# Performance work log

Hardware: AMD Instinct MI355X
Metric: run time of the kernel (lower is better)

The kernel has to match this reference:

```python
import jax, jax.numpy as jnp
import numpy as np

N = 10000      # num_nodes
E = 640000     # num_edges
IN = 512       # in_channels
H = 7          # GCNConv hidden/out dim (hard-coded in module)


def _glorot(key, shape):
    s = np.sqrt(6.0 / (shape[0] + shape[1])).astype(np.float32)
    return jax.random.uniform(key, shape, jnp.float32, -s, s)


def setup_inputs() -> dict:
    key = jax.random.key(0)
    k = jax.random.split(key, 6)
    x = jax.random.normal(k[0], (N, IN), jnp.float32)
    edge_index = jax.random.randint(k[1], (2, E), 0, N, dtype=jnp.int32)
    edge_attr = jax.random.uniform(k[2], (E, 1), jnp.float32)
    adj = jnp.zeros((N, N), jnp.float32)  # unused by forward, per original API
    W1 = _glorot(k[3], (IN, H))
    b1 = jnp.zeros((H,), jnp.float32)
    W2 = _glorot(k[4], (H, H))
    b2 = jnp.zeros((H,), jnp.float32)
    return {"x": x, "edge_index": edge_index, "edge_attr": edge_attr,
            "adj": adj, "W1": W1, "b1": b1, "W2": W2, "b2": b2}


def _gcn_layer(x, row, col, ew, W, b):
    n = x.shape[0]
    # add self-loops (improved=False -> loop weight 1)
    loop = jnp.arange(n, dtype=row.dtype)
    row_f = jnp.concatenate([row, loop])
    col_f = jnp.concatenate([col, loop])
    ew_f = jnp.concatenate([ew, jnp.ones((n,), x.dtype)])
    # symmetric degree normalization: deg from scatter_add on row
    deg = jax.ops.segment_sum(ew_f, row_f, num_segments=n)
    deg_inv = jnp.where(deg > 0, deg ** -0.5, 0.0).astype(x.dtype)
    norm = deg_inv[row_f] * ew_f * deg_inv[col_f]          # [E+N]
    h = x @ W                                              # [n, out]
    out = jax.ops.segment_sum(norm[:, None] * h[col_f], row_f, num_segments=n)
    return out + b


def reference(x, edge_index, edge_attr, adj, W1, b1, W2, b2):
    row, col = edge_index[0], edge_index[1]
    ew = edge_attr.reshape(-1)
    h = _gcn_layer(x, row, col, ew, W1, b1)
    h = _gcn_layer(h, row, col, ew, W2, b2)
    reg = jnp.zeros((1,), x.dtype)
    return h, reg
```

## Files before the change

kernel.cpp:

```cpp
#include <hip/hip_runtime.h>

#define NN   10000
#define NE   640000
#define IC   512
#define H    7
#define HP   8
#define NCH  256
#define CE   (NE / NCH)
#define RG   250
#define RN   40
#define CAP  3072
#define MMB  256
#define GN   32
#define NGB  ((NN + GN - 1) / GN)

__device__ __forceinline__ float wave_sum(float v) {
    #pragma unroll
    for (int off = 32; off; off >>= 1) v += __shfl_xor(v, off);
    return v;
}

__device__ __forceinline__ float group16_sum(float v) {
    #pragma unroll
    for (int off = 1; off < 16; off <<= 1) v += __shfl_xor(v, off);
    return v;
}

__global__ __launch_bounds__(1024) void k_bucket_mm1(
    const int* __restrict__ row, const int* __restrict__ col,
    const float* __restrict__ ew, const float* __restrict__ x,
    const float* __restrict__ W1, int* __restrict__ ghist,
    int* __restrict__ goffs, int2* __restrict__ gbuf2,
    float* __restrict__ h1)
{
    __shared__ int   lhist[RG];
    __shared__ int   loffs[RG];
    __shared__ int   lcur[RG];
    __shared__ int2  st[CE];
    __shared__ float wls[IC * H];
    const int tid = threadIdx.x;

    if (blockIdx.x < NCH) {
        const int base = blockIdx.x * CE;
        if (tid < RG) lhist[tid] = 0;
        __syncthreads();
        int ex[3]; float ef[3];
        #pragma unroll
        for (int k = 0; k < 3; ++k) {
            const int i = tid + k * 1024;
            ex[k] = -1;
            if (i < CE) {
                const int e = base + i;
                const int r = row[e], c = col[e];
                const int rg = r / RN, rl = r - rg * RN;
                ex[k] = c | (rl << 14) | (rg << 20);
                ef[k] = ew[e];
                atomicAdd(&lhist[rg], 1);
            }
        }
        __syncthreads();
        if (tid < 64) {
            const int ln = tid;
            int t4[4]; int s4 = 0;
            #pragma unroll
            for (int k = 0; k < 4; ++k) {
                const int j = ln * 4 + k;
                t4[k] = (j < RG) ? lhist[j] : 0;
                s4 += t4[k];
            }
            int s = s4;
            #pragma unroll
            for (int off = 1; off < 64; off <<= 1) {
                const int t = __shfl_up(s, off);
                if (ln >= off) s += t;
            }
            int run = s - s4;
            #pragma unroll
            for (int k = 0; k < 4; ++k) {
                const int j = ln * 4 + k;
                if (j < RG) { loffs[j] = run; lcur[j] = run; }
                run += t4[k];
            }
        }
        __syncthreads();
        #pragma unroll
        for (int k = 0; k < 3; ++k) {
            if (ex[k] >= 0) {
                const int pos = atomicAdd(&lcur[ex[k] >> 20], 1);
                st[pos] = make_int2(ex[k], __float_as_int(ef[k]));
            }
        }
        __syncthreads();
        #pragma unroll
        for (int k = 0; k < 3; ++k) {
            const int i = tid + k * 1024;
            if (i < CE) gbuf2[base + i] = st[i];
        }
        if (tid < RG) {
            ghist[blockIdx.x * RG + tid] = lhist[tid];
            goffs[blockIdx.x * RG + tid] = loffs[tid];
        }
    } else {
        for (int i = tid; i < IC * H; i += 1024) wls[i] = W1[i];
        __syncthreads();
        const int wv = tid >> 6, ln = tid & 63;
        const int rb = (blockIdx.x - NCH) * RN;
        for (int r0 = wv; r0 < RN; r0 += 16) {
            const int r = rb + r0;
            if (r >= NN) break;
            const float4* xr4 = (const float4*)(x + (size_t)r * IC);
            const float4 a0 = xr4[ln * 2], a1 = xr4[ln * 2 + 1];
            const float e8[8] = {a0.x, a0.y, a0.z, a0.w, a1.x, a1.y, a1.z, a1.w};
            const float* wb = &wls[ln * 8 * H];
            float acc[H] = {};
            #pragma unroll
            for (int m = 0; m < 8; ++m)
                #pragma unroll
                for (int c = 0; c < H; ++c) acc[c] += e8[m] * wb[m * H + c];
            #pragma unroll
            for (int c = 0; c < H; ++c) {
                const float v = wave_sum(acc[c]);
                if (ln == 0) h1[r * HP + c] = v;
            }
            if (ln == 0) h1[r * HP + 7] = 0.0f;
        }
    }
}

__global__ __launch_bounds__(1024) void k_sort_deg_g1(
    const int* __restrict__ ghist, const int* __restrict__ goffs,
    const int2* __restrict__ gbuf2, const float* __restrict__ h1,
    float* __restrict__ dinv, float* __restrict__ g1,
    int2* __restrict__ nseg, int2* __restrict__ gbuf)
{
    __shared__ int2  staged[CAP];
    __shared__ int2  st2[CAP];
    __shared__ int   ccnt[NCH];
    __shared__ int   coff[NCH];
    __shared__ int   total_s;
    __shared__ int   lhist[RN];
    __shared__ float ldeg[RN];
    __shared__ int   loffs[RN];
    __shared__ int   lcur[RN];
    __shared__ float ldv[RN];
    const int tid = threadIdx.x, b = blockIdx.x;

    if (tid < NCH) ccnt[tid] = ghist[tid * RG + b];
    if (tid >= 256 && tid < 256 + RN) { lhist[tid - 256] = 0; ldeg[tid - 256] = 0.0f; }
    __syncthreads();
    if (tid < 64) {
        const int ln = tid;
        int t4[4]; int s4 = 0;
        #pragma unroll
        for (int k = 0; k < 4; ++k) { t4[k] = ccnt[ln * 4 + k]; s4 += t4[k]; }
        int s = s4;
        #pragma unroll
        for (int off = 1; off < 64; off <<= 1) {
            const int t = __shfl_up(s, off);
            if (ln >= off) s += t;
        }
        int run = s - s4;
        #pragma unroll
        for (int k = 0; k < 4; ++k) { coff[ln * 4 + k] = run; run += t4[k]; }
        if (ln == 63) total_s = run;
    }
    __syncthreads();
    {
        const int c = tid >> 2;
        const int cn = ccnt[c], co = coff[c];
        const int src = c * CE + goffs[c * RG + b];
        for (int i = tid & 3; i < cn; i += 4) staged[co + i] = gbuf2[src + i];
    }
    __syncthreads();
    const int cnt = total_s;
    int2 ed[3];
    #pragma unroll
    for (int k = 0; k < 3; ++k) {
        const int i = tid + k * 1024;
        ed[k] = make_int2(-1, 0);
        if (i < cnt) {
            ed[k] = staged[i];
            const int rl = (ed[k].x >> 14) & 63;
            atomicAdd(&lhist[rl], 1);
            atomicAdd(&ldeg[rl], __int_as_float(ed[k].y));
        }
    }
    __syncthreads();
    if (tid < 64) {
        int v = (tid < RN) ? lhist[tid] : 0;
        int s = v;
        #pragma unroll
        for (int off = 1; off < 64; off <<= 1) {
            const int t = __shfl_up(s, off);
            if (tid >= off) s += t;
        }
        if (tid < RN) { loffs[tid] = s - v; lcur[tid] = s - v; }
    } else if (tid >= 64 && tid < 64 + RN) {
        ldv[tid - 64] = rsqrtf(1.0f + ldeg[tid - 64]);
    }
    __syncthreads();
    #pragma unroll
    for (int k = 0; k < 3; ++k) {
        if (ed[k].x >= 0) {
            const int rl = (ed[k].x >> 14) & 63;
            const int pos = atomicAdd(&lcur[rl], 1);
            st2[pos] = ed[k];
        }
    }
    __syncthreads();
    #pragma unroll
    for (int k = 0; k < 3; ++k) {
        const int i = tid + k * 1024;
        if (i < cnt) gbuf[(size_t)b * CAP + i] = st2[i];
    }
    if (tid < RN) {
        dinv[b * RN + tid] = ldv[tid];
        nseg[b * RN + tid] = make_int2(loffs[tid], lhist[tid]);
    }
    if (tid < RN * HP) {
        const int n = tid >> 3;
        g1[(size_t)(b * RN) * HP + tid] = ldv[n] * h1[(size_t)(b * RN) * HP + tid];
    }
}

template <bool FUSE_MM2>
__global__ __launch_bounds__(512) void k_gather(
    const int2* __restrict__ gbuf, const int2* __restrict__ nseg,
    const float* __restrict__ dinv, const float* __restrict__ g,
    const float* __restrict__ bias, const float* __restrict__ W2,
    float* __restrict__ out)
{
    __shared__ float asum[GN][HP];
    __shared__ float vals[GN][HP];
    __shared__ float ldv[GN];
    __shared__ float w2[H * H];
    __shared__ float bb[H];
    const int tid = threadIdx.x, b = blockIdx.x;
    const int gid = tid >> 4, q = tid & 15;
    const int gn = b * GN + gid;
    if (!FUSE_MM2 && b == 0 && tid == 511) out[(size_t)NN * H] = 0.0f;
    if (tid < GN && b * GN + tid < NN) ldv[tid] = dinv[b * GN + tid];
    if (FUSE_MM2 && tid >= 64 && tid < 64 + H * H) w2[tid - 64] = W2[tid - 64];
    if (tid >= 128 && tid < 128 + H) bb[tid - 128] = bias[tid - 128];
    __syncthreads();
    if (gn < NN) {
        const int2 seg = nseg[gn];
        const int2* bk = gbuf + (size_t)(gn / RN) * CAP;
        const int kend = seg.x + seg.y;
        float acc[H] = {};
        for (int k = seg.x + q; k < kend; k += 32) {
            const int k2i = k + 16;
            const int2 e0 = bk[k];
            const int2 e1 = bk[k2i < kend ? k2i : k];
            const float w0 = __int_as_float(e0.y);
            const float w1 = (k2i < kend) ? __int_as_float(e1.y) : 0.0f;
            const float4* p0 = (const float4*)(g + (size_t)(e0.x & 16383) * HP);
            const float4* p1 = (const float4*)(g + (size_t)(e1.x & 16383) * HP);
            const float4 lo0 = p0[0], hi0 = p0[1];
            const float4 lo1 = p1[0], hi1 = p1[1];
            acc[0] += w0 * lo0.x + w1 * lo1.x;
            acc[1] += w0 * lo0.y + w1 * lo1.y;
            acc[2] += w0 * lo0.z + w1 * lo1.z;
            acc[3] += w0 * lo0.w + w1 * lo1.w;
            acc[4] += w0 * hi0.x + w1 * hi1.x;
            acc[5] += w0 * hi0.y + w1 * hi1.y;
            acc[6] += w0 * hi0.z + w1 * hi1.z;
        }
        #pragma unroll
        for (int j = 0; j < H; ++j) {
            const float s = group16_sum(acc[j]);
            if (q == 0) asum[gid][j] = s;
        }
    }
    __syncthreads();
    if (tid < GN * H) {
        const int n = tid / H, k = tid - n * H;
        const int node = b * GN + n;
        if (node < NN)
            vals[n][k] = ldv[n] * (asum[n][k] + g[(size_t)node * HP + k]) + bb[k];
    }
    __syncthreads();
    if (tid < GN * H) {
        const int n = tid / H, k = tid - n * H;
        const int node = b * GN + n;
        if (node < NN) {
            if (FUSE_MM2) {
                float o = 0.0f;
                #pragma unroll
                for (int j = 0; j < H; ++j) o += vals[n][j] * w2[j * H + k];
                out[(size_t)node * HP + k] = ldv[n] * o;
            } else {
                out[(size_t)node * H + k] = vals[n][k];
            }
        }
    }
    if (FUSE_MM2 && tid >= 256 && tid < 256 + GN) {
        const int node = b * GN + (tid - 256);
        if (node < NN) out[(size_t)node * HP + 7] = 0.0f;
    }
}

extern "C" void kernel_launch(void* const* d_in, const int* in_sizes, int n_in,
                              void* d_out, int out_size, void* d_ws, size_t ws_size,
                              hipStream_t stream) {
    const float* x  = (const float*)d_in[0];
    const int*   ei = (const int*)d_in[1];
    const float* ea = (const float*)d_in[2];
    const float* W1 = (const float*)d_in[4];
    const float* b1 = (const float*)d_in[5];
    const float* W2 = (const float*)d_in[6];
    const float* b2 = (const float*)d_in[7];
    float* out = (float*)d_out;

    char* p = (char*)d_ws;
    int* ghist = (int*)p;         p += sizeof(int) * NCH * RG;
    int* goffs = (int*)p;         p += sizeof(int) * NCH * RG;
    int2* gbuf2 = (int2*)p;       p += sizeof(int2) * NE;
    int2* gbuf = (int2*)p;        p += sizeof(int2) * RG * CAP;
    int2* nseg = (int2*)p;        p += sizeof(int2) * NN;
    float* h1 = (float*)p;        p += sizeof(float) * NN * HP;
    float* g1 = (float*)p;        p += sizeof(float) * NN * HP;
    float* g2 = (float*)p;        p += sizeof(float) * NN * HP;
    float* dinv = (float*)p;      p += sizeof(float) * NN;

    const int* row = ei;
    const int* col = ei + NE;

    k_bucket_mm1<<<NCH + MMB, 1024, 0, stream>>>(row, col, ea, x, W1,
                                                 ghist, goffs, gbuf2, h1);
    k_sort_deg_g1<<<RG, 1024, 0, stream>>>(ghist, goffs, gbuf2, h1,
                                           dinv, g1, nseg, gbuf);
    k_gather<true><<<NGB, 512, 0, stream>>>(gbuf, nseg, dinv, g1, b1, W2, g2);
    k_gather<false><<<NGB, 512, 0, stream>>>(gbuf, nseg, dinv, g2, b2, nullptr, out);
}
```

Baseline: 47.84 us.

## Move layer-1 matmul into sort kernel and pack edges as 32-bit col+fp16 weight

The x@W1 projection moves out of the bucketing kernel into the per-row-group sort kernel. Each block computes its 40 rows into shared memory and scales them by dinv directly, so the h1 global round trip goes away. The sorted edge buffer is packed into 32 bits (14-bit column plus fp16 weight) instead of int2, and staged memory is reused. This halves the edge bytes the two gather kernels read, at the cost of fp16 rounding of edge weights. It also serialises the matmul behind bucketing instead of running them concurrently.

```diff
diff --git a/kernel.cpp b/kernel.cpp
--- a/kernel.cpp
+++ b/kernel.cpp
@@ -1,4 +1,5 @@
 #include <hip/hip_runtime.h>
+#include <hip/hip_fp16.h>
 
 #define NN   10000
 #define NE   640000
@@ -10,7 +11,6 @@
 #define RG   250
 #define RN   40
 #define CAP  3072
-#define MMB  256
 #define GN   32
 #define NGB  ((NN + GN - 1) / GN)
 
@@ -26,88 +26,128 @@
     return v;
 }
 
-__global__ __launch_bounds__(1024) void k_bucket_mm1(
+__global__ __launch_bounds__(1024) void k_bucket(
     const int* __restrict__ row, const int* __restrict__ col,
-    const float* __restrict__ ew, const float* __restrict__ x,
-    const float* __restrict__ W1, int* __restrict__ ghist,
-    int* __restrict__ goffs, int2* __restrict__ gbuf2,
-    float* __restrict__ h1)
+    const float* __restrict__ ew, int* __restrict__ ghist,
+    int* __restrict__ goffs, int2* __restrict__ gbuf2)
 {
     __shared__ int   lhist[RG];
     __shared__ int   loffs[RG];
     __shared__ int   lcur[RG];
     __shared__ int2  st[CE];
+    const int tid = threadIdx.x;
+    const int base = blockIdx.x * CE;
+    if (tid < RG) lhist[tid] = 0;
+    __syncthreads();
+    int ex[3]; float ef[3];
+    #pragma unroll
+    for (int k = 0; k < 3; ++k) {
+        const int i = tid + k * 1024;
+        ex[k] = -1;
+        if (i < CE) {
+            const int e = base + i;
+            const int r = row[e], c = col[e];
+            const int rg = r / RN, rl = r - rg * RN;
+            ex[k] = c | (rl << 14) | (rg << 20);
+            ef[k] = ew[e];
+            atomicAdd(&lhist[rg], 1);
+        }
+    }
+    __syncthreads();
+    if (tid < 64) {
+        const int ln = tid;
+        int t4[4]; int s4 = 0;
+        #pragma unroll
+        for (int k = 0; k < 4; ++k) {
+            const int j = ln * 4 + k;
+            t4[k] = (j < RG) ? lhist[j] : 0;
+            s4 += t4[k];
+        }
+        int s = s4;
+        #pragma unroll
+        for (int off = 1; off < 64; off <<= 1) {
+            const int t = __shfl_up(s, off);
+            if (ln >= off) s += t;
+        }
+        int run = s - s4;
+        #pragma unroll
+        for (int k = 0; k < 4; ++k) {
+            const int j = ln * 4 + k;
+            if (j < RG) { loffs[j] = run; lcur[j] = run; }
+            run += t4[k];
+        }
+    }
+    __syncthreads();
+    #pragma unroll
+    for (int k = 0; k < 3; ++k) {
+        if (ex[k] >= 0) {
+            const int pos = atomicAdd(&lcur[ex[k] >> 20], 1);
+            st[pos] = make_int2(ex[k], __float_as_int(ef[k]));
+        }
+    }
+    __syncthreads();
+    #pragma unroll
+    for (int k = 0; k < 3; ++k) {
+        const int i = tid + k * 1024;
+        if (i < CE) gbuf2[base + i] = st[i];
+    }
+    if (tid < RG) {
+        ghist[blockIdx.x * RG + tid] = lhist[tid];
+        goffs[blockIdx.x * RG + tid] = loffs[tid];
+    }
+}
+
+__global__ __launch_bounds__(1024) void k_stage_sort_mm1(
+    const int* __restrict__ ghist, const int* __restrict__ goffs,
+    const int2* __restrict__ gbuf2, const float* __restrict__ x,
+    const float* __restrict__ W1, float* __restrict__ dinv,
+    float* __restrict__ g1, int2* __restrict__ nseg,
+    unsigned int* __restrict__ gbuf)
+{
+    __shared__ int2  staged[CAP];
     __shared__ float wls[IC * H];
-    const int tid = threadIdx.x;
-
-    if (blockIdx.x < NCH) {
-        const int base = blockIdx.x * CE;
-        if (tid < RG) lhist[tid] = 0;
-        __syncthreads();
-        int ex[3]; float ef[3];
-        #pragma unroll
-        for (int k = 0; k < 3; ++k) {
-            const int i = tid + k * 1024;
-            ex[k] = -1;
-            if (i < CE) {
-                const int e = base + i;
-                const int r = row[e], c = col[e];
-                const int rg = r / RN, rl = r - rg * RN;
-                ex[k] = c | (rl << 14) | (rg << 20);
-                ef[k] = ew[e];
-                atomicAdd(&lhist[rg], 1);
-            }
-        }
-        __syncthreads();
-        if (tid < 64) {
-            const int ln = tid;
-            int t4[4]; int s4 = 0;
-            #pragma unroll
-            for (int k = 0; k < 4; ++k) {
-                const int j = ln * 4 + k;
-                t4[k] = (j < RG) ? lhist[j] : 0;
-                s4 += t4[k];
-            }
-            int s = s4;
-            #pragma unroll
-            for (int off = 1; off < 64; off <<= 1) {
-                const int t = __shfl_up(s, off);
-                if (ln >= off) s += t;
-            }
-            int run = s - s4;
-            #pragma unroll
-            for (int k = 0; k < 4; ++k) {
-                const int j = ln * 4 + k;
-                if (j < RG) { loffs[j] = run; lcur[j] = run; }
-                run += t4[k];
-            }
-        }
-        __syncthreads();
-        #pragma unroll
-        for (int k = 0; k < 3; ++k) {
-            if (ex[k] >= 0) {
-                const int pos = atomicAdd(&lcur[ex[k] >> 20], 1);
-                st[pos] = make_int2(ex[k], __float_as_int(ef[k]));
-            }
-        }
-        __syncthreads();
-        #pragma unroll
-        for (int k = 0; k < 3; ++k) {
-            const int i = tid + k * 1024;
-            if (i < CE) gbuf2[base + i] = st[i];
-        }
-        if (tid < RG) {
-            ghist[blockIdx.x * RG + tid] = lhist[tid];
-            goffs[blockIdx.x * RG + tid] = loffs[tid];
-        }
-    } else {
-        for (int i = tid; i < IC * H; i += 1024) wls[i] = W1[i];
-        __syncthreads();
-        const int wv = tid >> 6, ln = tid & 63;
-        const int rb = (blockIdx.x - NCH) * RN;
+    __shared__ int   ccnt[NCH];
+    __shared__ int   coff[NCH];
+    __shared__ int   total_s;
+    __shared__ int   lhist[RN];
+    __shared__ float ldeg[RN];
+    __shared__ int   loffs[RN];
+    __shared__ int   lcur[RN];
+    __shared__ float ldv[RN];
+    __shared__ float htile[RN][HP];
+    const int tid = threadIdx.x, b = blockIdx.x;
+    const int wv = tid >> 6, ln = tid & 63;
+
+    if (tid < NCH) ccnt[tid] = ghist[tid * RG + b];
+    if (tid >= 256 && tid < 256 + RN) { lhist[tid - 256] = 0; ldeg[tid - 256] = 0.0f; }
+    for (int i = tid; i < IC * H; i += 1024) wls[i] = W1[i];
+    __syncthreads();
+    if (tid < 64) {
+        const int ln0 = tid;
+        int t4[4]; int s4 = 0;
+        #pragma unroll
+        for (int k = 0; k < 4; ++k) { t4[k] = ccnt[ln0 * 4 + k]; s4 += t4[k]; }
+        int s = s4;
+        #pragma unroll
+        for (int off = 1; off < 64; off <<= 1) {
+            const int t = __shfl_up(s, off);
+            if (ln0 >= off) s += t;
+        }
+        int run = s - s4;
+        #pragma unroll
+        for (int k = 0; k < 4; ++k) { coff[ln0 * 4 + k] = run; run += t4[k]; }
+        if (ln0 == 63) total_s = run;
+    }
+    __syncthreads();
+    {
+        const int c = tid >> 2;
+        const int cn = ccnt[c], co = coff[c];
+        const int src = c * CE + goffs[c * RG + b];
+        for (int i = tid & 3; i < cn; i += 4) staged[co + i] = gbuf2[src + i];
+    }
+    {
         for (int r0 = wv; r0 < RN; r0 += 16) {
-            const int r = rb + r0;
-            if (r >= NN) break;
+            const int r = b * RN + r0;
             const float4* xr4 = (const float4*)(x + (size_t)r * IC);
             const float4 a0 = xr4[ln * 2], a1 = xr4[ln * 2 + 1];
             const float e8[8] = {a0.x, a0.y, a0.z, a0.w, a1.x, a1.y, a1.z, a1.w};
@@ -116,60 +156,14 @@
             #pragma unroll
             for (int m = 0; m < 8; ++m)
                 #pragma unroll
-                for (int c = 0; c < H; ++c) acc[c] += e8[m] * wb[m * H + c];
+                for (int c2 = 0; c2 < H; ++c2) acc[c2] += e8[m] * wb[m * H + c2];
             #pragma unroll
-            for (int c = 0; c < H; ++c) {
-                const float v = wave_sum(acc[c]);
-                if (ln == 0) h1[r * HP + c] = v;
+            for (int c2 = 0; c2 < H; ++c2) {
+                const float v = wave_sum(acc[c2]);
+                if (ln == 0) htile[r0][c2] = v;
             }
-            if (ln == 0) h1[r * HP + 7] = 0.0f;
-        }
-    }
-}
-
-__global__ __launch_bounds__(1024) void k_sort_deg_g1(
-    const int* __restrict__ ghist, const int* __restrict__ goffs,
-    const int2* __restrict__ gbuf2, const float* __restrict__ h1,
-    float* __restrict__ dinv, float* __restrict__ g1,
-    int2* __restrict__ nseg, int2* __restrict__ gbuf)
-{
-    __shared__ int2  staged[CAP];
-    __shared__ int2  st2[CAP];
-    __shared__ int   ccnt[NCH];
-    __shared__ int   coff[NCH];
-    __shared__ int   total_s;
-    __shared__ int   lhist[RN];
-    __shared__ float ldeg[RN];
-    __shared__ int   loffs[RN];
-    __shared__ int   lcur[RN];
-    __shared__ float ldv[RN];
-    const int tid = threadIdx.x, b = blockIdx.x;
-
-    if (tid < NCH) ccnt[tid] = ghist[tid * RG + b];
-    if (tid >= 256 && tid < 256 + RN) { lhist[tid - 256] = 0; ldeg[tid - 256] = 0.0f; }
-    __syncthreads();
-    if (tid < 64) {
-        const int ln = tid;
-        int t4[4]; int s4 = 0;
-        #pragma unroll
-        for (int k = 0; k < 4; ++k) { t4[k] = ccnt[ln * 4 + k]; s4 += t4[k]; }
-        int s = s4;
-        #pragma unroll
-        for (int off = 1; off < 64; off <<= 1) {
-            const int t = __shfl_up(s, off);
-            if (ln >= off) s += t;
-        }
-        int run = s - s4;
-        #pragma unroll
-        for (int k = 0; k < 4; ++k) { coff[ln * 4 + k] = run; run += t4[k]; }
-        if (ln == 63) total_s = run;
-    }
-    __syncthreads();
-    {
-        const int c = tid >> 2;
-        const int cn = ccnt[c], co = coff[c];
-        const int src = c * CE + goffs[c * RG + b];
-        for (int i = tid & 3; i < cn; i += 4) staged[co + i] = gbuf2[src + i];
+            if (ln == 0) htile[r0][7] = 0.0f;
+        }
     }
     __syncthreads();
     const int cnt = total_s;
@@ -199,19 +193,22 @@
         ldv[tid - 64] = rsqrtf(1.0f + ldeg[tid - 64]);
     }
     __syncthreads();
+    unsigned int* stp = (unsigned int*)staged;
     #pragma unroll
     for (int k = 0; k < 3; ++k) {
         if (ed[k].x >= 0) {
             const int rl = (ed[k].x >> 14) & 63;
             const int pos = atomicAdd(&lcur[rl], 1);
-            st2[pos] = ed[k];
+            const unsigned short wb16 =
+                __half_as_ushort(__float2half_rn(__int_as_float(ed[k].y)));
+            stp[pos] = (unsigned int)(ed[k].x & 16383) | ((unsigned int)wb16 << 16);
         }
     }
     __syncthreads();
     #pragma unroll
     for (int k = 0; k < 3; ++k) {
         const int i = tid + k * 1024;
-        if (i < cnt) gbuf[(size_t)b * CAP + i] = st2[i];
+        if (i < cnt) gbuf[(size_t)b * CAP + i] = stp[i];
     }
     if (tid < RN) {
         dinv[b * RN + tid] = ldv[tid];
@@ -219,13 +216,13 @@
     }
     if (tid < RN * HP) {
         const int n = tid >> 3;
-        g1[(size_t)(b * RN) * HP + tid] = ldv[n] * h1[(size_t)(b * RN) * HP + tid];
+        g1[(size_t)(b * RN) * HP + tid] = ldv[n] * htile[n][tid & 7];
     }
 }
 
 template <bool FUSE_MM2>
 __global__ __launch_bounds__(512) void k_gather(
-    const int2* __restrict__ gbuf, const int2* __restrict__ nseg,
+    const unsigned int* __restrict__ gbuf, const int2* __restrict__ nseg,
     const float* __restrict__ dinv, const float* __restrict__ g,
     const float* __restrict__ bias, const float* __restrict__ W2,
     float* __restrict__ out)
@@ -245,17 +242,18 @@
     __syncthreads();
     if (gn < NN) {
         const int2 seg = nseg[gn];
-        const int2* bk = gbuf + (size_t)(gn / RN) * CAP;
+        const unsigned int* bk = gbuf + (size_t)(gn / RN) * CAP;
         const int kend = seg.x + seg.y;
         float acc[H] = {};
         for (int k = seg.x + q; k < kend; k += 32) {
             const int k2i = k + 16;
-            const int2 e0 = bk[k];
-            const int2 e1 = bk[k2i < kend ? k2i : k];
-            const float w0 = __int_as_float(e0.y);
-            const float w1 = (k2i < kend) ? __int_as_float(e1.y) : 0.0f;
-            const float4* p0 = (const float4*)(g + (size_t)(e0.x & 16383) * HP);
-            const float4* p1 = (const float4*)(g + (size_t)(e1.x & 16383) * HP);
+            const unsigned int e0 = bk[k];
+            const unsigned int e1 = bk[k2i < kend ? k2i : k];
+            const float w0 = __half2float(__ushort_as_half((unsigned short)(e0 >> 16)));
+            float w1 = __half2float(__ushort_as_half((unsigned short)(e1 >> 16)));
+            if (k2i >= kend) w1 = 0.0f;
+            const float4* p0 = (const float4*)(g + (size_t)(e0 & 16383u) * HP);
+            const float4* p1 = (const float4*)(g + (size_t)(e1 & 16383u) * HP);
             const float4 lo0 = p0[0], hi0 = p0[1];
             const float4 lo1 = p1[0], hi1 = p1[1];
             acc[0] += w0 * lo0.x + w1 * lo1.x;
@@ -313,23 +311,21 @@
     float* out = (float*)d_out;
 
     char* p = (char*)d_ws;
-    int* ghist = (int*)p;         p += sizeof(int) * NCH * RG;
-    int* goffs = (int*)p;         p += sizeof(int) * NCH * RG;
-    int2* gbuf2 = (int2*)p;       p += sizeof(int2) * NE;
-    int2* gbuf = (int2*)p;        p += sizeof(int2) * RG * CAP;
-    int2* nseg = (int2*)p;        p += sizeof(int2) * NN;
-    float* h1 = (float*)p;        p += sizeof(float) * NN * HP;
-    float* g1 = (float*)p;        p += sizeof(float) * NN * HP;
-    float* g2 = (float*)p;        p += sizeof(float) * NN * HP;
-    float* dinv = (float*)p;      p += sizeof(float) * NN;
+    int* ghist = (int*)p;                 p += sizeof(int) * NCH * RG;
+    int* goffs = (int*)p;                 p += sizeof(int) * NCH * RG;
+    int2* gbuf2 = (int2*)p;               p += sizeof(int2) * NE;
+    unsigned int* gbuf = (unsigned int*)p; p += sizeof(unsigned int) * RG * CAP;
+    int2* nseg = (int2*)p;                p += sizeof(int2) * NN;
+    float* g1 = (float*)p;                p += sizeof(float) * NN * HP;
+    float* g2 = (float*)p;                p += sizeof(float) * NN * HP;
+    float* dinv = (float*)p;              p += sizeof(float) * NN;
 
     const int* row = ei;
     const int* col = ei + NE;
 
-    k_bucket_mm1<<<NCH + MMB, 1024, 0, stream>>>(row, col, ea, x, W1,
-                                                 ghist, goffs, gbuf2, h1);
-    k_sort_deg_g1<<<RG, 1024, 0, stream>>>(ghist, goffs, gbuf2, h1,
-                                           dinv, g1, nseg, gbuf);
+    k_bucket<<<NCH, 1024, 0, stream>>>(row, col, ea, ghist, goffs, gbuf2);
+    k_stage_sort_mm1<<<RG, 1024, 0, stream>>>(ghist, goffs, gbuf2, x, W1,
+                                              dinv, g1, nseg, gbuf);
     k_gather<true><<<NGB, 512, 0, stream>>>(gbuf, nseg, dinv, g1, b1, W2, g2);
     k_gather<false><<<NGB, 512, 0, stream>>>(gbuf, nseg, dinv, g2, b2, nullptr, out);
 }
```

Result: faster. 45.01 us (-5.9%).
